# Kernel tuning notes

Hardware: AMD Instinct MI355X
Metric: run time of the kernel (lower is better)

Reference implementation:

```python
import jax, jax.numpy as jnp
import numpy as np

NUM_HEADS = 32
NUM_KV_HEADS = 8
HEAD_DIM = 64
Q_MULT = NUM_HEADS // NUM_KV_HEADS  # 4
WINDOW = 128
BATCH = 2
SEQ = 2048


def setup_inputs() -> dict:
    key = jax.random.key(0)
    k1, k2, k3 = jax.random.split(key, 3)
    Q = jax.random.normal(k1, (BATCH, SEQ, NUM_HEADS * HEAD_DIM), dtype=jnp.float32)
    K = jax.random.normal(k2, (BATCH, SEQ, NUM_KV_HEADS * HEAD_DIM), dtype=jnp.float32)
    V = jax.random.normal(k3, (BATCH, SEQ, NUM_KV_HEADS * HEAD_DIM), dtype=jnp.float32)
    sinks = jnp.zeros((NUM_HEADS,), dtype=jnp.float32)
    return {"Q": Q, "K": K, "V": V, "sinks": sinks}


def _sdpa_single(Qb, Kb, Vb, sinks):
    # Qb: (n, num_heads*head_dim); Kb/Vb: (n, num_kv_heads*head_dim)
    n = Qb.shape[0]
    Q = Qb.reshape(n, NUM_KV_HEADS, Q_MULT, HEAD_DIM)
    K = Kb.reshape(n, NUM_KV_HEADS, HEAD_DIM)
    V = Vb.reshape(n, NUM_KV_HEADS, HEAD_DIM)
    sm_scale = 1.0 / np.sqrt(HEAD_DIM)
    # NOTE: the reference torch sdpa() builds S (sinks) but never adds it to QK;
    # we faithfully reproduce that (sinks unused in the math).
    q_idx = jnp.arange(n)[:, None]
    k_idx = jnp.arange(n)[None, :]
    # causal AND within sliding window of 128
    allowed = (k_idx <= q_idx) & (k_idx > q_idx - WINDOW)
    mask = jnp.where(allowed, jnp.float32(0.0), -jnp.inf)
    # scores: (h, m, q, k) where h = kv head, m = q_mult (GQA expand of K is implicit via einsum)
    QK = jnp.einsum('qhmd,khd->hmqk', Q, K) * sm_scale + mask[None, None, :, :]
    W = jax.nn.softmax(QK, axis=-1)
    attn = jnp.einsum('hmqk,khd->qhmd', W, V)
    return attn.reshape(n, -1)


def reference(Q, K, V, sinks):
    return jax.vmap(_sdpa_single, in_axes=(0, 0, 0, None))(Q, K, V, sinks)
```

## Files before the change

kernel.cpp:

```cpp
#include <hip/hip_runtime.h>


constexpr int NKV = 8, QM = 4, WIN = 128, BATCH = 2, SEQ = 2048;
constexpr int QSTRIDE = 2048, KSTRIDE = 512, HD = 64;

typedef __attribute__((ext_vector_type(8))) __bf16 bf16x8;
typedef __attribute__((ext_vector_type(8))) short short8_t;
typedef __attribute__((ext_vector_type(4))) float f32x4;

__device__ __forceinline__ short f2bf(float f) {
    unsigned u = __float_as_uint(f);
    u += 0x7FFF + ((u >> 16) & 1u);
    return (short)(u >> 16);
}

__device__ __forceinline__ f32x4 mfma16(short8_t a, short8_t b, f32x4 c) {
    return __builtin_amdgcn_mfma_f32_16x16x32_bf16(
        __builtin_bit_cast(bf16x8, a), __builtin_bit_cast(bf16x8, b), c, 0, 0, 0);
}

__global__ __launch_bounds__(256, 4)
void swa_mfma4(const float* __restrict__ Q, const float* __restrict__ K,
               const float* __restrict__ V, float* __restrict__ O)
{
    __shared__ __align__(16) short Ksh[32][72];
    __shared__ __align__(16) short Vsh[64][40];
    __shared__ __align__(16) short Psh[4][16][40];

    const int tid  = threadIdx.x;
    const int lane = tid & 63;
    const int w    = tid >> 6;
    const int col  = lane & 15;
    const int quad = lane >> 4;

    int blk = blockIdx.x;
    const int b   = blk & 1;
    const int kvh = (blk >> 1) & 7;
    const int qg  = blk >> 4;
    const int q0  = qg * 32;
    const int h   = kvh * QM + w;

    const float* QA = Q + ((size_t)(b * SEQ + q0 + col) * QSTRIDE + h * HD);
    const float* QB = QA + (size_t)16 * QSTRIDE;
    short8_t aqA0, aqA1, aqB0, aqB1;
    {
        float4 f0 = *(const float4*)(QA + quad * 8);
        float4 f1 = *(const float4*)(QA + quad * 8 + 4);
        float4 g0 = *(const float4*)(QA + 32 + quad * 8);
        float4 g1 = *(const float4*)(QA + 32 + quad * 8 + 4);
        aqA0 = short8_t{f2bf(f0.x), f2bf(f0.y), f2bf(f0.z), f2bf(f0.w),
                        f2bf(f1.x), f2bf(f1.y), f2bf(f1.z), f2bf(f1.w)};
        aqA1 = short8_t{f2bf(g0.x), f2bf(g0.y), f2bf(g0.z), f2bf(g0.w),
                        f2bf(g1.x), f2bf(g1.y), f2bf(g1.z), f2bf(g1.w)};
        f0 = *(const float4*)(QB + quad * 8);
        f1 = *(const float4*)(QB + quad * 8 + 4);
        g0 = *(const float4*)(QB + 32 + quad * 8);
        g1 = *(const float4*)(QB + 32 + quad * 8 + 4);
        aqB0 = short8_t{f2bf(f0.x), f2bf(f0.y), f2bf(f0.z), f2bf(f0.w),
                        f2bf(f1.x), f2bf(f1.y), f2bf(f1.z), f2bf(f1.w)};
        aqB1 = short8_t{f2bf(g0.x), f2bf(g0.y), f2bf(g0.z), f2bf(g0.w),
                        f2bf(g1.x), f2bf(g1.y), f2bf(g1.z), f2bf(g1.w)};
    }

    const float* Kb = K + ((size_t)b * SEQ * KSTRIDE + (size_t)kvh * HD);
    const float* Vb = V + ((size_t)b * SEQ * KSTRIDE + (size_t)kvh * HD);

    f32x4 oA0 = {0.f,0.f,0.f,0.f}, oA1 = oA0, oA2 = oA0, oA3 = oA0;
    f32x4 oB0 = oA0, oB1 = oA0, oB2 = oA0, oB3 = oA0;
    float liA[4] = {0.f,0.f,0.f,0.f}, liB[4] = {0.f,0.f,0.f,0.f};

    const int krow = tid >> 3, kseg = tid & 7;
    const int vd = tid & 63, vkg = tid >> 6;

    for (int t = 0; t < 5; ++t) {
        const int kbase = q0 - WIN + 32 * t;
        if (kbase < 0) continue;

        __syncthreads();
        {
            const float* s = Kb + (size_t)(kbase + krow) * KSTRIDE + kseg * 8;
            const float4 a = *(const float4*)s;
            const float4 c = *(const float4*)(s + 4);
            *(short8_t*)&Ksh[krow][kseg * 8] =
                short8_t{f2bf(a.x), f2bf(a.y), f2bf(a.z), f2bf(a.w),
                         f2bf(c.x), f2bf(c.y), f2bf(c.z), f2bf(c.w)};
        }
        {
            const float* sv = Vb + (size_t)(kbase + vkg * 8) * KSTRIDE + vd;
            short vv[8];
#pragma unroll
            for (int j = 0; j < 8; ++j) vv[j] = f2bf(sv[(size_t)j * KSTRIDE]);
            *(short8_t*)&Vsh[vd][vkg * 8] =
                short8_t{vv[0], vv[1], vv[2], vv[3], vv[4], vv[5], vv[6], vv[7]};
        }
        __syncthreads();

        const short8_t b0lo = *(const short8_t*)&Ksh[col][quad * 8];
        const short8_t b0hi = *(const short8_t*)&Ksh[col][quad * 8 + 32];
        const short8_t b1lo = *(const short8_t*)&Ksh[16 + col][quad * 8];
        const short8_t b1hi = *(const short8_t*)&Ksh[16 + col][quad * 8 + 32];
        const short8_t vb0  = *(const short8_t*)&Vsh[col][quad * 8];
        const short8_t vb1  = *(const short8_t*)&Vsh[16 + col][quad * 8];
        const short8_t vb2  = *(const short8_t*)&Vsh[32 + col][quad * 8];
        const short8_t vb3  = *(const short8_t*)&Vsh[48 + col][quad * 8];

        {
            f32x4 s0 = {0.f,0.f,0.f,0.f}, s1 = s0;
            s0 = mfma16(aqA0, b0lo, s0); s0 = mfma16(aqA1, b0hi, s0);
            if (t < 4) { s1 = mfma16(aqA0, b1lo, s1); s1 = mfma16(aqA1, b1hi, s1); }
#pragma unroll
            for (int r = 0; r < 4; ++r) {
                const int rr = quad * 4 + r;
                float a0 = fmaf(s0[r], 0.125f, -8.0f);
                float a1 = fmaf(s1[r], 0.125f, -8.0f);
                if (t == 0) a0 = (col > rr)  ? a0 : -1e30f;
                if (t == 4) { a0 = (col <= rr) ? a0 : -1e30f; a1 = -1e30f; }
                const float p0 = __expf(a0), p1 = __expf(a1);
                liA[r] += p0 + p1;
                Psh[w][rr][col]      = f2bf(p0);
                Psh[w][rr][16 + col] = f2bf(p1);
            }
            const short8_t pa = *(const short8_t*)&Psh[w][col][quad * 8];
            oA0 = mfma16(pa, vb0, oA0); oA1 = mfma16(pa, vb1, oA1);
            oA2 = mfma16(pa, vb2, oA2); oA3 = mfma16(pa, vb3, oA3);
        }

        {
            f32x4 s0 = {0.f,0.f,0.f,0.f}, s1 = s0;
            if (t > 0) { s0 = mfma16(aqB0, b0lo, s0); s0 = mfma16(aqB1, b0hi, s0); }
            s1 = mfma16(aqB0, b1lo, s1); s1 = mfma16(aqB1, b1hi, s1);
#pragma unroll
            for (int r = 0; r < 4; ++r) {
                const int rr = quad * 4 + r;
                float a0 = fmaf(s0[r], 0.125f, -8.0f);
                float a1 = fmaf(s1[r], 0.125f, -8.0f);
                if (t == 0) { a0 = -1e30f; a1 = (col > rr) ? a1 : -1e30f; }
                if (t == 4) a1 = (col <= rr) ? a1 : -1e30f;
                const float p0 = __expf(a0), p1 = __expf(a1);
                liB[r] += p0 + p1;
                Psh[w][rr][col]      = f2bf(p0);
                Psh[w][rr][16 + col] = f2bf(p1);
            }
            const short8_t pa = *(const short8_t*)&Psh[w][col][quad * 8];
            oB0 = mfma16(pa, vb0, oB0); oB1 = mfma16(pa, vb1, oB1);
            oB2 = mfma16(pa, vb2, oB2); oB3 = mfma16(pa, vb3, oB3);
        }
    }

    float* OA = O + ((size_t)(b * SEQ + q0) * QSTRIDE + h * HD);
    float* OB = OA + (size_t)16 * QSTRIDE;
#pragma unroll
    for (int r = 0; r < 4; ++r) {
        float lA = liA[r], lB = liB[r];
        lA += __shfl_xor(lA, 1); lA += __shfl_xor(lA, 2);
        lA += __shfl_xor(lA, 4); lA += __shfl_xor(lA, 8);
        lB += __shfl_xor(lB, 1); lB += __shfl_xor(lB, 2);
        lB += __shfl_xor(lB, 4); lB += __shfl_xor(lB, 8);
        const float iA = 1.0f / lA, iB = 1.0f / lB;
        const size_t row = (size_t)(quad * 4 + r) * QSTRIDE;
        OA[row + col]      = oA0[r] * iA;
        OA[row + 16 + col] = oA1[r] * iA;
        OA[row + 32 + col] = oA2[r] * iA;
        OA[row + 48 + col] = oA3[r] * iA;
        OB[row + col]      = oB0[r] * iB;
        OB[row + 16 + col] = oB1[r] * iB;
        OB[row + 32 + col] = oB2[r] * iB;
        OB[row + 48 + col] = oB3[r] * iB;
    }
}

extern "C" void kernel_launch(void* const* d_in, const int* in_sizes, int n_in,
                              void* d_out, int out_size, void* d_ws, size_t ws_size,
                              hipStream_t stream) {
    const float* Q = (const float*)d_in[0];
    const float* K = (const float*)d_in[1];
    const float* V = (const float*)d_in[2];
    float* O = (float*)d_out;

    dim3 grid(BATCH * NKV * (SEQ / 32));
    dim3 block(256);
    swa_mfma4<<<grid, block, 0, stream>>>(Q, K, V, O);
}
```

Baseline: 105.3 us.

## Prefetch next K/V tile into registers and use exp2 with folded scale

After: 130.2 us. +23.7%, slower.

```diff
diff --git a/kernel.cpp b/kernel.cpp
--- a/kernel.cpp
+++ b/kernel.cpp
@@ -19,8 +19,11 @@
         __builtin_bit_cast(bf16x8, a), __builtin_bit_cast(bf16x8, b), c, 0, 0, 0);
 }
 
+constexpr float C1f = 0.18033688011112042f;
+constexpr float C0f = -11.541560327111707f;
+
 __global__ __launch_bounds__(256, 4)
-void swa_mfma4(const float* __restrict__ Q, const float* __restrict__ K,
+void swa_mfma6(const float* __restrict__ Q, const float* __restrict__ K,
                const float* __restrict__ V, float* __restrict__ O)
 {
     __shared__ __align__(16) short Ksh[32][72];
@@ -55,7 +58,7 @@
         f0 = *(const float4*)(QB + quad * 8);
         f1 = *(const float4*)(QB + quad * 8 + 4);
         g0 = *(const float4*)(QB + 32 + quad * 8);
-        g1 = *(const float4*)(QB + 32 + quad * 8 + 4);
+        g1 = *(const float4*)(QB + 36 + quad * 8);
         aqB0 = short8_t{f2bf(f0.x), f2bf(f0.y), f2bf(f0.z), f2bf(f0.w),
                         f2bf(f1.x), f2bf(f1.y), f2bf(f1.z), f2bf(f1.w)};
         aqB1 = short8_t{f2bf(g0.x), f2bf(g0.y), f2bf(g0.z), f2bf(g0.w),
@@ -72,29 +75,7 @@
     const int krow = tid >> 3, kseg = tid & 7;
     const int vd = tid & 63, vkg = tid >> 6;
 
-    for (int t = 0; t < 5; ++t) {
-        const int kbase = q0 - WIN + 32 * t;
-        if (kbase < 0) continue;
-
-        __syncthreads();
-        {
-            const float* s = Kb + (size_t)(kbase + krow) * KSTRIDE + kseg * 8;
-            const float4 a = *(const float4*)s;
-            const float4 c = *(const float4*)(s + 4);
-            *(short8_t*)&Ksh[krow][kseg * 8] =
-                short8_t{f2bf(a.x), f2bf(a.y), f2bf(a.z), f2bf(a.w),
-                         f2bf(c.x), f2bf(c.y), f2bf(c.z), f2bf(c.w)};
-        }
-        {
-            const float* sv = Vb + (size_t)(kbase + vkg * 8) * KSTRIDE + vd;
-            short vv[8];
-#pragma unroll
-            for (int j = 0; j < 8; ++j) vv[j] = f2bf(sv[(size_t)j * KSTRIDE]);
-            *(short8_t*)&Vsh[vd][vkg * 8] =
-                short8_t{vv[0], vv[1], vv[2], vv[3], vv[4], vv[5], vv[6], vv[7]};
-        }
-        __syncthreads();
-
+    auto compute = [&](int t) {
         const short8_t b0lo = *(const short8_t*)&Ksh[col][quad * 8];
         const short8_t b0hi = *(const short8_t*)&Ksh[col][quad * 8 + 32];
         const short8_t b1lo = *(const short8_t*)&Ksh[16 + col][quad * 8];
@@ -104,46 +85,90 @@
         const short8_t vb2  = *(const short8_t*)&Vsh[32 + col][quad * 8];
         const short8_t vb3  = *(const short8_t*)&Vsh[48 + col][quad * 8];
 
-        {
+        auto tile = [&](short8_t a0f, short8_t a1f, float* li, f32x4* o,
+                        int m0, int m1) {
+            const bool L0 = (m0 >= 0) && (m0 <= 8);
+            const bool L1 = (m1 >= 0) && (m1 <= 8);
             f32x4 s0 = {0.f,0.f,0.f,0.f}, s1 = s0;
-            s0 = mfma16(aqA0, b0lo, s0); s0 = mfma16(aqA1, b0hi, s0);
-            if (t < 4) { s1 = mfma16(aqA0, b1lo, s1); s1 = mfma16(aqA1, b1hi, s1); }
+            if (L0) { s0 = mfma16(a0f, b0lo, s0); s0 = mfma16(a1f, b0hi, s0); }
+            if (L1) { s1 = mfma16(a0f, b1lo, s1); s1 = mfma16(a1f, b1hi, s1); }
 #pragma unroll
             for (int r = 0; r < 4; ++r) {
                 const int rr = quad * 4 + r;
-                float a0 = fmaf(s0[r], 0.125f, -8.0f);
-                float a1 = fmaf(s1[r], 0.125f, -8.0f);
-                if (t == 0) a0 = (col > rr)  ? a0 : -1e30f;
-                if (t == 4) { a0 = (col <= rr) ? a0 : -1e30f; a1 = -1e30f; }
-                const float p0 = __expf(a0), p1 = __expf(a1);
-                liA[r] += p0 + p1;
+                float a0 = fmaf(s0[r], C1f, C0f);
+                float a1 = fmaf(s1[r], C1f, C0f);
+                if (m0 == 8) a0 = (col > rr)  ? a0 : -1e30f;
+                if (m0 == 0) a0 = (col <= rr) ? a0 : -1e30f;
+                if (m1 == 8) a1 = (col > rr)  ? a1 : -1e30f;
+                if (m1 == 0) a1 = (col <= rr) ? a1 : -1e30f;
+                const float p0 = L0 ? exp2f(a0) : 0.f;
+                const float p1 = L1 ? exp2f(a1) : 0.f;
+                li[r] += p0 + p1;
                 Psh[w][rr][col]      = f2bf(p0);
                 Psh[w][rr][16 + col] = f2bf(p1);
             }
             const short8_t pa = *(const short8_t*)&Psh[w][col][quad * 8];
-            oA0 = mfma16(pa, vb0, oA0); oA1 = mfma16(pa, vb1, oA1);
-            oA2 = mfma16(pa, vb2, oA2); oA3 = mfma16(pa, vb3, oA3);
+            o[0] = mfma16(pa, vb0, o[0]); o[1] = mfma16(pa, vb1, o[1]);
+            o[2] = mfma16(pa, vb2, o[2]); o[3] = mfma16(pa, vb3, o[3]);
+        };
+
+        f32x4 oAarr[4] = {oA0, oA1, oA2, oA3};
+        f32x4 oBarr[4] = {oB0, oB1, oB2, oB3};
+        tile(aqA0, aqA1, liA, oAarr, 8 - 2 * t,     7 - 2 * t);
+        tile(aqB0, aqB1, liB, oBarr, 9 - 2 * t,     8 - 2 * t);
+        oA0 = oAarr[0]; oA1 = oAarr[1]; oA2 = oAarr[2]; oA3 = oAarr[3];
+        oB0 = oBarr[0]; oB1 = oBarr[1]; oB2 = oBarr[2]; oB3 = oBarr[3];
+    };
+
+    auto stage_write = [&](const float4& ka, const float4& kc, const float* vv) {
+        *(short8_t*)&Ksh[krow][kseg * 8] =
+            short8_t{f2bf(ka.x), f2bf(ka.y), f2bf(ka.z), f2bf(ka.w),
+                     f2bf(kc.x), f2bf(kc.y), f2bf(kc.z), f2bf(kc.w)};
+        *(short8_t*)&Vsh[vd][vkg * 8] =
+            short8_t{f2bf(vv[0]), f2bf(vv[1]), f2bf(vv[2]), f2bf(vv[3]),
+                     f2bf(vv[4]), f2bf(vv[5]), f2bf(vv[6]), f2bf(vv[7])};
+    };
+
+    if (q0 >= WIN) {
+        const float* kp = Kb + (size_t)(q0 - WIN + krow) * KSTRIDE + kseg * 8;
+        const float* vp = Vb + (size_t)(q0 - WIN + vkg * 8) * KSTRIDE + vd;
+        float4 ka = *(const float4*)kp;
+        float4 kc = *(const float4*)(kp + 4);
+        float vv[8];
+#pragma unroll
+        for (int jj = 0; jj < 8; ++jj) vv[jj] = vp[(size_t)jj * KSTRIDE];
+
+#pragma unroll
+        for (int t = 0; t < 5; ++t) {
+            __syncthreads();
+            stage_write(ka, kc, vv);
+            if (t < 4) {
+                kp += 32 * KSTRIDE; vp += 32 * KSTRIDE;
+                ka = *(const float4*)kp;
+                kc = *(const float4*)(kp + 4);
+#pragma unroll
+                for (int jj = 0; jj < 8; ++jj) vv[jj] = vp[(size_t)jj * KSTRIDE];
+            }
+            __syncthreads();
+            compute(t);
         }
-
-        {
-            f32x4 s0 = {0.f,0.f,0.f,0.f}, s1 = s0;
-            if (t > 0) { s0 = mfma16(aqB0, b0lo, s0); s0 = mfma16(aqB1, b0hi, s0); }
-            s1 = mfma16(aqB0, b1lo, s1); s1 = mfma16(aqB1, b1hi, s1);
-#pragma unroll
-            for (int r = 0; r < 4; ++r) {
-                const int rr = quad * 4 + r;
-                float a0 = fmaf(s0[r], 0.125f, -8.0f);
-                float a1 = fmaf(s1[r], 0.125f, -8.0f);
-                if (t == 0) { a0 = -1e30f; a1 = (col > rr) ? a1 : -1e30f; }
-                if (t == 4) a1 = (col <= rr) ? a1 : -1e30f;
-                const float p0 = __expf(a0), p1 = __expf(a1);
-                liB[r] += p0 + p1;
-                Psh[w][rr][col]      = f2bf(p0);
-                Psh[w][rr][16 + col] = f2bf(p1);
+    } else {
+        for (int t = 0; t < 5; ++t) {
+            const int kbase = q0 - WIN + 32 * t;
+            if (kbase < 0) continue;
+            __syncthreads();
+            {
+                const float* s = Kb + (size_t)(kbase + krow) * KSTRIDE + kseg * 8;
+                const float4 a = *(const float4*)s;
+                const float4 c = *(const float4*)(s + 4);
+                float vv[8];
+                const float* sv = Vb + (size_t)(kbase + vkg * 8) * KSTRIDE + vd;
+#pragma unroll
+                for (int jj = 0; jj < 8; ++jj) vv[jj] = sv[(size_t)jj * KSTRIDE];
+                stage_write(a, c, vv);
             }
-            const short8_t pa = *(const short8_t*)&Psh[w][col][quad * 8];
-            oB0 = mfma16(pa, vb0, oB0); oB1 = mfma16(pa, vb1, oB1);
-            oB2 = mfma16(pa, vb2, oB2); oB3 = mfma16(pa, vb3, oB3);
+            __syncthreads();
+            compute(t);
         }
     }
 
@@ -179,5 +204,5 @@
 
     dim3 grid(BATCH * NKV * (SEQ / 32));
     dim3 block(256);
-    swa_mfma4<<<grid, block, 0, stream>>>(Q, K, V, O);
-}
+    swa_mfma6<<<grid, block, 0, stream>>>(Q, K, V, O);
+}
```

## Double-buffer K/V tiles with register prefetch and use exp2 with folded constants

Applied to the files above, without the earlier changes.

New measurement: 110.8 us. +5.3%, slower.

```diff
diff --git a/kernel.cpp b/kernel.cpp
--- a/kernel.cpp
+++ b/kernel.cpp
@@ -19,12 +19,15 @@
         __builtin_bit_cast(bf16x8, a), __builtin_bit_cast(bf16x8, b), c, 0, 0, 0);
 }
 
+constexpr float C1f = 0.18033688011112042f;
+constexpr float C0f = -11.541560327111707f;
+
 __global__ __launch_bounds__(256, 4)
-void swa_mfma4(const float* __restrict__ Q, const float* __restrict__ K,
+void swa_mfma8(const float* __restrict__ Q, const float* __restrict__ K,
                const float* __restrict__ V, float* __restrict__ O)
 {
-    __shared__ __align__(16) short Ksh[32][72];
-    __shared__ __align__(16) short Vsh[64][40];
+    __shared__ __align__(16) short Ksh[2][32][72];
+    __shared__ __align__(16) short Vsh[2][64][40];
     __shared__ __align__(16) short Psh[4][16][40];
 
     const int tid  = threadIdx.x;
@@ -58,6 +61,7 @@
         g1 = *(const float4*)(QB + 32 + quad * 8 + 4);
         aqB0 = short8_t{f2bf(f0.x), f2bf(f0.y), f2bf(f0.z), f2bf(f0.w),
                         f2bf(f1.x), f2bf(f1.y), f2bf(f1.z), f2bf(f1.w)};
+        aqB0 = aqB0;
         aqB1 = short8_t{f2bf(g0.x), f2bf(g0.y), f2bf(g0.z), f2bf(g0.w),
                         f2bf(g1.x), f2bf(g1.y), f2bf(g1.z), f2bf(g1.w)};
     }
@@ -72,37 +76,43 @@
     const int krow = tid >> 3, kseg = tid & 7;
     const int vd = tid & 63, vkg = tid >> 6;
 
-    for (int t = 0; t < 5; ++t) {
-        const int kbase = q0 - WIN + 32 * t;
-        if (kbase < 0) continue;
+    const int t_start = (q0 >= WIN) ? 0 : ((WIN - q0) >> 5);
 
-        __syncthreads();
-        {
-            const float* s = Kb + (size_t)(kbase + krow) * KSTRIDE + kseg * 8;
-            const float4 a = *(const float4*)s;
-            const float4 c = *(const float4*)(s + 4);
-            *(short8_t*)&Ksh[krow][kseg * 8] =
-                short8_t{f2bf(a.x), f2bf(a.y), f2bf(a.z), f2bf(a.w),
-                         f2bf(c.x), f2bf(c.y), f2bf(c.z), f2bf(c.w)};
-        }
-        {
-            const float* sv = Vb + (size_t)(kbase + vkg * 8) * KSTRIDE + vd;
-            short vv[8];
-#pragma unroll
-            for (int j = 0; j < 8; ++j) vv[j] = f2bf(sv[(size_t)j * KSTRIDE]);
-            *(short8_t*)&Vsh[vd][vkg * 8] =
-                short8_t{vv[0], vv[1], vv[2], vv[3], vv[4], vv[5], vv[6], vv[7]};
+    const float* kp = Kb + (size_t)(q0 - WIN + 32 * t_start + krow) * KSTRIDE + kseg * 8;
+    const float* vp = Vb + (size_t)(q0 - WIN + 32 * t_start + vkg * 8) * KSTRIDE + vd;
+    float4 ka = *(const float4*)kp;
+    float4 kc = *(const float4*)(kp + 4);
+    float pv0 = vp[0],           pv1 = vp[KSTRIDE],     pv2 = vp[2 * KSTRIDE],
+          pv3 = vp[3 * KSTRIDE], pv4 = vp[4 * KSTRIDE], pv5 = vp[5 * KSTRIDE],
+          pv6 = vp[6 * KSTRIDE], pv7 = vp[7 * KSTRIDE];
+
+#pragma unroll 1
+    for (int t = t_start; t < 5; ++t) {
+        const int buf = t & 1;
+        *(short8_t*)&Ksh[buf][krow][kseg * 8] =
+            short8_t{f2bf(ka.x), f2bf(ka.y), f2bf(ka.z), f2bf(ka.w),
+                     f2bf(kc.x), f2bf(kc.y), f2bf(kc.z), f2bf(kc.w)};
+        *(short8_t*)&Vsh[buf][vd][vkg * 8] =
+            short8_t{f2bf(pv0), f2bf(pv1), f2bf(pv2), f2bf(pv3),
+                     f2bf(pv4), f2bf(pv5), f2bf(pv6), f2bf(pv7)};
+        if (t < 4) {
+            kp += 32 * KSTRIDE; vp += 32 * KSTRIDE;
+            ka = *(const float4*)kp;
+            kc = *(const float4*)(kp + 4);
+            pv0 = vp[0];           pv1 = vp[KSTRIDE];     pv2 = vp[2 * KSTRIDE];
+            pv3 = vp[3 * KSTRIDE]; pv4 = vp[4 * KSTRIDE]; pv5 = vp[5 * KSTRIDE];
+            pv6 = vp[6 * KSTRIDE]; pv7 = vp[7 * KSTRIDE];
         }
         __syncthreads();
 
-        const short8_t b0lo = *(const short8_t*)&Ksh[col][quad * 8];
-        const short8_t b0hi = *(const short8_t*)&Ksh[col][quad * 8 + 32];
-        const short8_t b1lo = *(const short8_t*)&Ksh[16 + col][quad * 8];
-        const short8_t b1hi = *(const short8_t*)&Ksh[16 + col][quad * 8 + 32];
-        const short8_t vb0  = *(const short8_t*)&Vsh[col][quad * 8];
-        const short8_t vb1  = *(const short8_t*)&Vsh[16 + col][quad * 8];
-        const short8_t vb2  = *(const short8_t*)&Vsh[32 + col][quad * 8];
-        const short8_t vb3  = *(const short8_t*)&Vsh[48 + col][quad * 8];
+        const short8_t b0lo = *(const short8_t*)&Ksh[buf][col][quad * 8];
+        const short8_t b0hi = *(const short8_t*)&Ksh[buf][col][quad * 8 + 32];
+        const short8_t b1lo = *(const short8_t*)&Ksh[buf][16 + col][quad * 8];
+        const short8_t b1hi = *(const short8_t*)&Ksh[buf][16 + col][quad * 8 + 32];
+        const short8_t vb0  = *(const short8_t*)&Vsh[buf][col][quad * 8];
+        const short8_t vb1  = *(const short8_t*)&Vsh[buf][16 + col][quad * 8];
+        const short8_t vb2  = *(const short8_t*)&Vsh[buf][32 + col][quad * 8];
+        const short8_t vb3  = *(const short8_t*)&Vsh[buf][48 + col][quad * 8];
 
         {
             f32x4 s0 = {0.f,0.f,0.f,0.f}, s1 = s0;
@@ -111,11 +121,12 @@
 #pragma unroll
             for (int r = 0; r < 4; ++r) {
                 const int rr = quad * 4 + r;
-                float a0 = fmaf(s0[r], 0.125f, -8.0f);
-                float a1 = fmaf(s1[r], 0.125f, -8.0f);
+                float a0 = fmaf(s0[r], C1f, C0f);
+                float a1 = fmaf(s1[r], C1f, C0f);
                 if (t == 0) a0 = (col > rr)  ? a0 : -1e30f;
                 if (t == 4) { a0 = (col <= rr) ? a0 : -1e30f; a1 = -1e30f; }
-                const float p0 = __expf(a0), p1 = __expf(a1);
+                const float p0 = exp2f(a0);
+                const float p1 = (t < 4) ? exp2f(a1) : 0.f;
                 liA[r] += p0 + p1;
                 Psh[w][rr][col]      = f2bf(p0);
                 Psh[w][rr][16 + col] = f2bf(p1);
@@ -132,11 +143,12 @@
 #pragma unroll
             for (int r = 0; r < 4; ++r) {
                 const int rr = quad * 4 + r;
-                float a0 = fmaf(s0[r], 0.125f, -8.0f);
-                float a1 = fmaf(s1[r], 0.125f, -8.0f);
-                if (t == 0) { a0 = -1e30f; a1 = (col > rr) ? a1 : -1e30f; }
+                float a0 = fmaf(s0[r], C1f, C0f);
+                float a1 = fmaf(s1[r], C1f, C0f);
+                if (t == 0) a1 = (col > rr) ? a1 : -1e30f;
                 if (t == 4) a1 = (col <= rr) ? a1 : -1e30f;
-                const float p0 = __expf(a0), p1 = __expf(a1);
+                const float p0 = (t > 0) ? exp2f(a0) : 0.f;
+                const float p1 = exp2f(a1);
                 liB[r] += p0 + p1;
                 Psh[w][rr][col]      = f2bf(p0);
                 Psh[w][rr][16 + col] = f2bf(p1);
@@ -179,5 +191,5 @@
 
     dim3 grid(BATCH * NKV * (SEQ / 32));
     dim3 block(256);
-    swa_mfma4<<<grid, block, 0, stream>>>(Q, K, V, O);
+    swa_mfma8<<<grid, block, 0, stream>>>(Q, K, V, O);
 }
```
